# Performance work log

Hardware: AMD Instinct MI355X
Metric: run time of the kernel (lower is better)

Reference implementation:

```python
import jax, jax.numpy as jnp
import numpy as np

LN_EPS = 1e-5


def _layernorm(x, g, b):
    m = jnp.mean(x, axis=-1, keepdims=True)
    v = jnp.mean((x - m) ** 2, axis=-1, keepdims=True)
    return (x - m) / jnp.sqrt(v + LN_EPS) * g + b


def _eigenstate_fft(log_decay, frequency, beta_r, beta_i):
    # beta_r, beta_i: [B, T, K]; log_decay, frequency: [K]
    B, T, K = beta_r.shape
    mag = jax.nn.sigmoid(log_decay)                       # [K]
    n = jnp.arange(T, dtype=beta_r.dtype)                 # [T]
    mag_pow = mag[None, :] ** n[:, None]                  # [T, K]
    phase = n[:, None] * frequency[None, :]               # [T, K]
    kern = mag_pow * (jnp.cos(phase) + 1j * jnp.sin(phase))  # complex [T, K]
    beta = beta_r + 1j * beta_i                           # [B, T, K]
    beta_p = jnp.pad(beta, ((0, 0), (0, T), (0, 0)))      # zero-pad to 2T
    kern_p = jnp.pad(kern, ((0, T), (0, 0)))
    c = jnp.fft.ifft(jnp.fft.fft(beta_p, axis=1) * jnp.fft.fft(kern_p, axis=0)[None], axis=1)[:, :T, :]
    return c.real.astype(beta_r.dtype), c.imag.astype(beta_r.dtype)


def setup_inputs() -> dict:
    key = jax.random.key(0)
    ks = jax.random.split(key, 12)
    B, T, D, K, H = 4, 4096, 1024, 64, 4
    Kh = K // H
    M = 4 * D
    f32 = jnp.float32
    inp = {
        "x": jax.random.normal(ks[0], (B, T, D), f32),
        "in_proj_w": jax.random.normal(ks[1], (2 * K, D), f32) / np.sqrt(D),
        "log_decay": jax.random.uniform(ks[2], (K,), f32, -3.0, -0.1),
        "frequency": jnp.linspace(0.0, 2 * np.pi * (1 - 1.0 / K), K, dtype=f32),
        "coupling": jnp.eye(Kh, dtype=f32)[None] + 0.01 * jax.random.normal(ks[3], (H, Kh, Kh), f32) / np.sqrt(Kh),
        "out_proj_w": jax.random.normal(ks[4], (D, 2 * K), f32) / np.sqrt(2 * K),
        "gate_w": jax.random.normal(ks[5], (D, D), f32) / np.sqrt(D),
        "gate_b": jnp.full((D,), -2.0, f32),
        "n1_g": jnp.ones((D,), f32),
        "n1_b": jnp.zeros((D,), f32),
        "n2_g": jnp.ones((D,), f32),
        "n2_b": jnp.zeros((D,), f32),
        "mlp_w1": jax.random.normal(ks[6], (M, D), f32) / np.sqrt(D),
        "mlp_b1": jnp.zeros((M,), f32),
        "mlp_w2": jax.random.normal(ks[7], (D, M), f32) / np.sqrt(M),
        "mlp_b2": jnp.zeros((D,), f32),
    }
    return inp


def reference(x, in_proj_w, log_decay, frequency, coupling, out_proj_w,
              gate_w, gate_b, n1_g, n1_b, n2_g, n2_b,
              mlp_w1, mlp_b1, mlp_w2, mlp_b2):
    B, T, D = x.shape
    H, Kh, _ = coupling.shape
    K = H * Kh
    xn = _layernorm(x, n1_g, n1_b)
    beta = jnp.einsum('btd,kd->btk', xn, in_proj_w)        # [B, T, 2K]
    br, bi = beta[..., :K], beta[..., K:]
    cr, ci = _eigenstate_fft(log_decay, frequency, br, bi)  # [B, T, K] each
    cr_h = cr.reshape(B, T, H, Kh)
    ci_h = ci.reshape(B, T, H, Kh)
    cr = jnp.einsum('hjk,bthk->bthj', coupling, cr_h).reshape(B, T, K)
    ci = jnp.einsum('hjk,bthk->bthj', coupling, ci_h).reshape(B, T, K)
    eig = jnp.concatenate([cr, ci], axis=-1)               # [B, T, 2K]
    out = jnp.einsum('btk,dk->btd', eig, out_proj_w)
    h = jax.nn.sigmoid(jnp.einsum('btd,ed->bte', xn, gate_w) + gate_b) * out
    x = x + h                                              # dropout = identity (eval)
    x2 = _layernorm(x, n2_g, n2_b)
    hid = jax.nn.silu(jnp.einsum('btd,md->btm', x2, mlp_w1) + mlp_b1)
    x = x + jnp.einsum('btm,dm->btd', hid, mlp_w2) + mlp_b2
    return x, eig
```

## Files before the change

### kernel.cpp

```cpp
#include <hip/hip_runtime.h>
#include <hip/hip_bf16.h>
#include <math.h>

#define BATCH 4
#define TLEN  4096
#define DDIM  1024
#define BT    16384

typedef __attribute__((ext_vector_type(8))) __bf16 bf16x8;
typedef __attribute__((ext_vector_type(4))) float  f32x4;

#define AS1 __attribute__((address_space(1)))
#define AS3 __attribute__((address_space(3)))

__device__ __forceinline__ short f2bf(float f) {
    union { float f; unsigned int i; } u; u.f = f;
    unsigned int r = u.i + 0x7FFF + ((u.i >> 16) & 1);
    return (short)(r >> 16);
}

__global__ void cvt_bf16_kernel(const float* __restrict__ in, short* __restrict__ out, int n4) {
    int i = blockIdx.x * blockDim.x + threadIdx.x;
    int stride = gridDim.x * blockDim.x;
    for (; i < n4; i += stride) {
        float4 v = ((const float4*)in)[i];
        short4 o = make_short4(f2bf(v.x), f2bf(v.y), f2bf(v.z), f2bf(v.w));
        ((short4*)out)[i] = o;
    }
}

__global__ __launch_bounds__(256) void ln_kernel(const float* __restrict__ x,
                                                 const float* __restrict__ g,
                                                 const float* __restrict__ b,
                                                 short* __restrict__ out) {
    __shared__ float red[8];
    __shared__ float mv[2];
    int row = blockIdx.x, tid = threadIdx.x;
    const float* xr = x + (size_t)row * DDIM;
    float4 v = *(const float4*)&xr[tid * 4];
    float s  = v.x + v.y + v.z + v.w;
    float s2 = v.x*v.x + v.y*v.y + v.z*v.z + v.w*v.w;
    for (int o = 32; o; o >>= 1) { s += __shfl_down(s, o); s2 += __shfl_down(s2, o); }
    int wave = tid >> 6, lane = tid & 63;
    if (lane == 0) { red[wave] = s; red[4 + wave] = s2; }
    __syncthreads();
    if (tid == 0) {
        float ts  = red[0] + red[1] + red[2] + red[3];
        float ts2 = red[4] + red[5] + red[6] + red[7];
        float m = ts * (1.f / DDIM);
        float var = ts2 * (1.f / DDIM) - m * m;
        mv[0] = m; mv[1] = rsqrtf(var + 1e-5f);
    }
    __syncthreads();
    float m = mv[0], r = mv[1];
    const float* vv = (const float*)&v;
    short o4[4];
    #pragma unroll
    for (int j = 0; j < 4; ++j) {
        int c = tid * 4 + j;
        o4[j] = f2bf((vv[j] - m) * r * g[c] + b[c]);
    }
    *(short4*)&out[(size_t)row * DDIM + tid * 4] = make_short4(o4[0], o4[1], o4[2], o4[3]);
}

#define EIG_TT 16
#define WIN 64
__global__ __launch_bounds__(256) void eig_kernel(const float* __restrict__ beta,
                                                  const float* __restrict__ log_decay,
                                                  const float* __restrict__ freq,
                                                  const float* __restrict__ coupling,
                                                  float* __restrict__ eig_f32,
                                                  short* __restrict__ eig_bf) {
    __shared__ float bsm[EIG_TT + WIN][128];
    __shared__ float csm[EIG_TT][128];
    __shared__ float psm[4][16][16];
    int tpb = TLEN / EIG_TT;
    int b   = blockIdx.x / tpb;
    int t0  = (blockIdx.x % tpb) * EIG_TT;
    int tid = threadIdx.x;

    for (int idx = tid; idx < (EIG_TT + WIN) * 32; idx += 256) {
        int r = idx >> 5, c4 = idx & 31;
        int t = t0 - WIN + r;
        float4 val = make_float4(0.f, 0.f, 0.f, 0.f);
        if (t >= 0) val = *(const float4*)&beta[((size_t)(b * TLEN + t)) * 128 + c4 * 4];
        *(float4*)&bsm[r][c4 * 4] = val;
    }
    for (int i = tid; i < 1024; i += 256) ((float*)psm)[i] = coupling[i];
    __syncthreads();

    int k = tid & 63;
    float mag = 1.f / (1.f + __expf(-log_decay[k]));
    float th  = freq[k];
    float lr = mag * cosf(th), li = mag * sinf(th);
    #pragma unroll
    for (int p = 0; p < 4; ++p) {
        int tl = (tid >> 6) + p * 4;
        float ar = 0.f, ai = 0.f;
        for (int s = WIN - 1; s >= 0; --s) {
            float br_ = bsm[tl + WIN - s][k];
            float bi_ = bsm[tl + WIN - s][64 + k];
            float nr = lr * ar - li * ai + br_;
            float ni = lr * ai + li * ar + bi_;
            ar = nr; ai = ni;
        }
        csm[tl][k] = ar; csm[tl][64 + k] = ai;
    }
    __syncthreads();

    #pragma unroll
    for (int p = 0; p < 8; ++p) {
        int idx = tid + p * 256;
        int c = idx & 127, tl = idx >> 7;
        int im = c >> 6, hj = c & 63, h = hj >> 4, j = hj & 15;
        float acc = 0.f;
        #pragma unroll
        for (int kk = 0; kk < 16; ++kk) acc += psm[h][j][kk] * csm[tl][im * 64 + h * 16 + kk];
        size_t o = ((size_t)(b * TLEN + t0 + tl)) * 128 + c;
        eig_f32[o] = acc;
        eig_bf[o]  = f2bf(acc);
    }
}

__global__ __launch_bounds__(256) void gemm_bt(const short* __restrict__ A,
                                               const short* __restrict__ Bt,
                                               float* __restrict__ C,
                                               int Ndim, int Kdim) {
    __shared__ short Asm[128 * 32];
    __shared__ short Bsm[128 * 32];
    int nb = Ndim >> 7;
    int bm = blockIdx.x / nb, bn = blockIdx.x % nb;
    int m0 = bm << 7, n0 = bn << 7;
    int tid = threadIdx.x, lane = tid & 63, wave = tid >> 6;
    int wr = wave >> 1, wc = wave & 1;
    f32x4 acc[4][4] = {};
    int ldrow = lane >> 2;
    int ldcol = (lane & 3) * 8;
    int frow = lane & 15, fch = lane >> 4;

    for (int k0 = 0; k0 < Kdim; k0 += 32) {
        #pragma unroll
        for (int r = 0; r < 2; ++r) {
            int chunk = wave * 2 + r;
            int row = chunk * 16 + ldrow;
            __builtin_amdgcn_global_load_lds(
                (const AS1 unsigned int*)(A + (size_t)(m0 + row) * Kdim + k0 + ldcol),
                (AS3 unsigned int*)(Asm + chunk * 512 + lane * 8), 16, 0, 0);
            __builtin_amdgcn_global_load_lds(
                (const AS1 unsigned int*)(Bt + (size_t)(n0 + row) * Kdim + k0 + ldcol),
                (AS3 unsigned int*)(Bsm + chunk * 512 + lane * 8), 16, 0, 0);
        }
        __syncthreads();
        bf16x8 af[4], bf[4];
        #pragma unroll
        for (int m = 0; m < 4; ++m) af[m] = *(const bf16x8*)&Asm[(wr * 64 + m * 16 + frow) * 32 + fch * 8];
        #pragma unroll
        for (int n = 0; n < 4; ++n) bf[n] = *(const bf16x8*)&Bsm[(wc * 64 + n * 16 + frow) * 32 + fch * 8];
        #pragma unroll
        for (int m = 0; m < 4; ++m)
            #pragma unroll
            for (int n = 0; n < 4; ++n)
                acc[m][n] = __builtin_amdgcn_mfma_f32_16x16x32_bf16(af[m], bf[n], acc[m][n], 0, 0, 0);
        __syncthreads();
    }
    #pragma unroll
    for (int m = 0; m < 4; ++m) {
        int row = m0 + wr * 64 + m * 16 + fch * 4;
        #pragma unroll
        for (int n = 0; n < 4; ++n) {
            int col = n0 + wc * 64 + n * 16 + frow;
            #pragma unroll
            for (int j = 0; j < 4; ++j)
                C[(size_t)(row + j) * Ndim + col] = acc[m][n][j];
        }
    }
}

enum { E_NONE = 0, E_GATEFUSE = 1, E_SILU_BF = 2, E_RES = 3 };

#define BARRIER do { asm volatile("" ::: "memory"); __builtin_amdgcn_s_barrier(); } while (0)

#define STAGE(src, grow0, tau_, ldsShortBase) do { \
    int _i = tid; \
    _Pragma("unroll") \
    for (int _r = 0; _r < 2; ++_r, _i += 512) { \
        int _row = _i >> 3, _slot = _i & 7; \
        const short* _gp = (src) + (size_t)((grow0) + _row) * Kdim + ((tau_) << 6) \
                           + ((_slot ^ (_row & 7)) << 3); \
        __builtin_amdgcn_global_load_lds((const AS1 unsigned int*)_gp, \
            (AS3 unsigned int*)(lds + (ldsShortBase) + _i * 8), 16, 0, 0); \
    } \
} while (0)

#define LOAD_A(Ab, mq) do { \
    af0 = *(const bf16x8*)((Ab) + (2*(mq))  *2048 + lrb + x0); \
    af1 = *(const bf16x8*)((Ab) + (2*(mq))  *2048 + lrb + x1); \
    af2 = *(const bf16x8*)((Ab) + (2*(mq)+1)*2048 + lrb + x0); \
    af3 = *(const bf16x8*)((Ab) + (2*(mq)+1)*2048 + lrb + x1); \
} while (0)

#define PHASE_MFMA(mA, mB) do { \
    _Pragma("unroll") \
    for (int n = 0; n < 4; ++n) { \
        acc[mA][n] = __builtin_amdgcn_mfma_f32_16x16x32_bf16(af0, bfrag[n][0], acc[mA][n], 0, 0, 0); \
        acc[mA][n] = __builtin_amdgcn_mfma_f32_16x16x32_bf16(af1, bfrag[n][1], acc[mA][n], 0, 0, 0); \
        acc[mB][n] = __builtin_amdgcn_mfma_f32_16x16x32_bf16(af2, bfrag[n][0], acc[mB][n], 0, 0, 0); \
        acc[mB][n] = __builtin_amdgcn_mfma_f32_16x16x32_bf16(af3, bfrag[n][1], acc[mB][n], 0, 0, 0); \
    } \
} while (0)

#define KTILE(Ab, Bb, pB, pN, tau_) do { \
    bf16x8 af0, af1, af2, af3; \
     \
    LOAD_A(Ab, 0); \
    _Pragma("unroll") \
    for (int n = 0; n < 4; ++n) { \
        bfrag[n][0] = *(const bf16x8*)((Bb) + n * 2048 + lrb + x0); \
        bfrag[n][1] = *(const bf16x8*)((Bb) + n * 2048 + lrb + x1); \
    } \
    if ((tau_) + 1 < NT) STAGE(A, m0 + 128, (tau_) + 1, (pN) + 8192); \
    BARRIER; \
    __builtin_amdgcn_s_setprio(1); \
    PHASE_MFMA(0, 1); \
    __builtin_amdgcn_s_setprio(0); \
    BARRIER; \
     \
    LOAD_A(Ab, 1); \
    if ((tau_) + 2 < NT) STAGE(Bt, n0, (tau_) + 2, (pB) + 16384); \
    BARRIER; \
    __builtin_amdgcn_s_setprio(1); \
    PHASE_MFMA(2, 3); \
    __builtin_amdgcn_s_setprio(0); \
    BARRIER; \
     \
    LOAD_A(Ab, 2); \
    if ((tau_) + 2 < NT) STAGE(Bt, n0 + 128, (tau_) + 2, (pB) + 16384 + 8192); \
    BARRIER; \
    __builtin_amdgcn_s_setprio(1); \
    PHASE_MFMA(4, 5); \
    __builtin_amdgcn_s_setprio(0); \
    BARRIER; \
     \
    LOAD_A(Ab, 3); \
    BARRIER; \
    __builtin_amdgcn_s_setprio(1); \
    PHASE_MFMA(6, 7); \
    __builtin_amdgcn_s_setprio(0); \
    if ((tau_) + 2 < NT) { \
        STAGE(A, m0, (tau_) + 2, (pB)); \
        asm volatile("s_waitcnt vmcnt(6)" ::: "memory"); \
    } else { \
        asm volatile("s_waitcnt vmcnt(0)" ::: "memory"); \
    } \
    BARRIER; \
} while (0)

template <int EPI>
__global__ __launch_bounds__(512, 2) void gemm256(const short* __restrict__ A,
                                                  const short* __restrict__ Bt,
                                                  void* __restrict__ C,
                                                  int Ndim, int Kdim,
                                                  const float* __restrict__ bias,
                                                  const float* __restrict__ res,
                                                  const float* __restrict__ xin,
                                                  const float* __restrict__ outp) {
    __shared__ short lds[65536];
    const int NT = Kdim >> 6;
    const int nb = Ndim >> 8;
    int nwg = gridDim.x;
    int wg  = blockIdx.x;
    int swz = (wg & 7) * (nwg >> 3) + (wg >> 3);
    int bm = swz / nb, bn = swz % nb;
    int m0 = bm << 8, n0 = bn << 8;
    int tid = threadIdx.x, lane = tid & 63, wave = tid >> 6;
    int wr = wave >> 2, wc = wave & 3;
    int frow = lane & 15, fch = lane >> 4;

    f32x4 acc[8][4] = {};
    bf16x8 bfrag[4][2];

    int lrb = frow * 128;
    int sx  = frow & 7;
    int x0  = (fch ^ sx) << 4;
    int x1  = ((fch + 4) ^ sx) << 4;

    const char* Ab0 = (const char*)lds + wr * 16384;
    const char* Bb0 = (const char*)lds + 32768 + (wc >> 1) * 16384 + (wc & 1) * 8192;
    const char* Ab1 = Ab0 + 65536;
    const char* Bb1 = Bb0 + 65536;

    STAGE(Bt, n0,       0, 16384);
    STAGE(Bt, n0 + 128, 0, 16384 + 8192);
    STAGE(A,  m0,       0, 0);
    STAGE(A,  m0 + 128, 0, 8192);
    if (NT > 1) {
        STAGE(Bt, n0,       1, 32768 + 16384);
        STAGE(Bt, n0 + 128, 1, 32768 + 16384 + 8192);
        STAGE(A,  m0,       1, 32768);
    }
    asm volatile("s_waitcnt vmcnt(6)" ::: "memory");
    BARRIER;

    for (int tau = 0; tau < NT; tau += 2) {
        KTILE(Ab0, Bb0, 0,     32768, tau);
        KTILE(Ab1, Bb1, 32768, 0,     tau + 1);
    }

    #pragma unroll
    for (int m = 0; m < 8; ++m) {
        int row = m0 + wr * 128 + m * 16 + fch * 4;
        #pragma unroll
        for (int n = 0; n < 4; ++n) {
            int col = n0 + wc * 64 + n * 16 + frow;
            #pragma unroll
            for (int j = 0; j < 4; ++j) {
                float v = acc[m][n][j];
                size_t o = (size_t)(row + j) * Ndim + col;
                if (EPI == E_NONE) {
                    ((float*)C)[o] = v;
                } else if (EPI == E_GATEFUSE) {
                    float t = v + bias[col];
                    float s = 1.f / (1.f + __expf(-t));
                    ((float*)C)[o] = xin[o] + s * outp[o];
                } else if (EPI == E_SILU_BF) {
                    float t = v + bias[col];
                    ((short*)C)[o] = f2bf(t / (1.f + __expf(-t)));
                } else {
                    ((float*)C)[o] = v + bias[col] + res[o];
                }
            }
        }
    }
}

extern "C" void kernel_launch(void* const* d_in, const int* in_sizes, int n_in,
                              void* d_out, int out_size, void* d_ws, size_t ws_size,
                              hipStream_t stream) {
    const float* x          = (const float*)d_in[0];
    const float* in_proj_w  = (const float*)d_in[1];
    const float* log_decay  = (const float*)d_in[2];
    const float* frequency  = (const float*)d_in[3];
    const float* coupling   = (const float*)d_in[4];
    const float* out_proj_w = (const float*)d_in[5];
    const float* gate_w     = (const float*)d_in[6];
    const float* gate_b     = (const float*)d_in[7];
    const float* n1_g       = (const float*)d_in[8];
    const float* n1_b       = (const float*)d_in[9];
    const float* n2_g       = (const float*)d_in[10];
    const float* n2_b       = (const float*)d_in[11];
    const float* mlp_w1     = (const float*)d_in[12];
    const float* mlp_b1     = (const float*)d_in[13];
    const float* mlp_w2     = (const float*)d_in[14];
    const float* mlp_b2     = (const float*)d_in[15];

    float* out_x   = (float*)d_out;
    float* out_eig = out_x + (size_t)BT * DDIM;

    char* ws = (char*)d_ws;
    short* w_inproj  = (short*)(ws + 0);
    short* w_outproj = (short*)(ws + 262144);
    short* w_gate    = (short*)(ws + 524288);
    short* w_1       = (short*)(ws + 2621440);
    short* w_2       = (short*)(ws + 11010048);
    short* xn        = (short*)(ws + 19398656);
    float* beta      = (float*)(ws + 52953088);
    short* eig_bf    = (short*)(ws + 61341696);
    short* hid       = (short*)(ws + 65536000);
    float* outp      = (float*)(ws + 132644864);

    cvt_bf16_kernel<<<64,   256, 0, stream>>>(in_proj_w,  w_inproj,  131072 / 4);
    cvt_bf16_kernel<<<64,   256, 0, stream>>>(out_proj_w, w_outproj, 131072 / 4);
    cvt_bf16_kernel<<<256,  256, 0, stream>>>(gate_w,     w_gate,    1048576 / 4);
    cvt_bf16_kernel<<<1024, 256, 0, stream>>>(mlp_w1,     w_1,       4194304 / 4);
    cvt_bf16_kernel<<<1024, 256, 0, stream>>>(mlp_w2,     w_2,       4194304 / 4);

    ln_kernel<<<BT, 256, 0, stream>>>(x, n1_g, n1_b, xn);

    gemm_bt<<<BT / 128, 256, 0, stream>>>(xn, w_inproj, beta, 128, 1024);

    eig_kernel<<<BATCH * (TLEN / EIG_TT), 256, 0, stream>>>(beta, log_decay, frequency, coupling, out_eig, eig_bf);

    gemm256<E_NONE><<<(BT / 256) * (1024 / 256), 512, 0, stream>>>(
        eig_bf, w_outproj, outp, 1024, 128, nullptr, nullptr, nullptr, nullptr);

    gemm256<E_GATEFUSE><<<(BT / 256) * (1024 / 256), 512, 0, stream>>>(
        xn, w_gate, out_x, 1024, 1024, gate_b, nullptr, x, outp);

    ln_kernel<<<BT, 256, 0, stream>>>(out_x, n2_g, n2_b, xn);

    gemm256<E_SILU_BF><<<(BT / 256) * (4096 / 256), 512, 0, stream>>>(
        xn, w_1, hid, 4096, 1024, mlp_b1, nullptr, nullptr, nullptr);

    gemm256<E_RES><<<(BT / 256) * (1024 / 256), 512, 0, stream>>>(
        hid, w_2, out_x, 1024, 4096, mlp_b2, out_x, nullptr, nullptr);
}
```

Measured before the change: 630.0 us.

## Double-buffer A fragments and drop intra-phase barriers in GEMM k-tile loop

Splits A-fragment register reads into two ping-pong sets so the next quarter's LDS reads are issued before the current MFMA phase runs. It removes the barrier that sat between each LDS read and its MFMA phase, halving the barriers per k-tile. The last quarter's MFMAs are moved after the final A stage issue. This adds register pressure and depends on correct LDS hazard ordering, since stage writes may now overlap reads of the same buffer region.

```diff
diff --git a/kernel.cpp b/kernel.cpp
--- a/kernel.cpp
+++ b/kernel.cpp
@@ -192,64 +192,56 @@
     } \
 } while (0)
 
-#define LOAD_A(Ab, mq) do { \
-    af0 = *(const bf16x8*)((Ab) + (2*(mq))  *2048 + lrb + x0); \
-    af1 = *(const bf16x8*)((Ab) + (2*(mq))  *2048 + lrb + x1); \
-    af2 = *(const bf16x8*)((Ab) + (2*(mq)+1)*2048 + lrb + x0); \
-    af3 = *(const bf16x8*)((Ab) + (2*(mq)+1)*2048 + lrb + x1); \
+#define RD_AF(F, Ab, mq) do { \
+    F[0] = *(const bf16x8*)((Ab) + (2*(mq))  *2048 + lrb + x0); \
+    F[1] = *(const bf16x8*)((Ab) + (2*(mq))  *2048 + lrb + x1); \
+    F[2] = *(const bf16x8*)((Ab) + (2*(mq)+1)*2048 + lrb + x0); \
+    F[3] = *(const bf16x8*)((Ab) + (2*(mq)+1)*2048 + lrb + x1); \
 } while (0)
 
-#define PHASE_MFMA(mA, mB) do { \
+#define MFMA_Q(mA, mB, F) do { \
+    __builtin_amdgcn_s_setprio(1); \
     _Pragma("unroll") \
     for (int n = 0; n < 4; ++n) { \
-        acc[mA][n] = __builtin_amdgcn_mfma_f32_16x16x32_bf16(af0, bfrag[n][0], acc[mA][n], 0, 0, 0); \
-        acc[mA][n] = __builtin_amdgcn_mfma_f32_16x16x32_bf16(af1, bfrag[n][1], acc[mA][n], 0, 0, 0); \
-        acc[mB][n] = __builtin_amdgcn_mfma_f32_16x16x32_bf16(af2, bfrag[n][0], acc[mB][n], 0, 0, 0); \
-        acc[mB][n] = __builtin_amdgcn_mfma_f32_16x16x32_bf16(af3, bfrag[n][1], acc[mB][n], 0, 0, 0); \
+        acc[mA][n] = __builtin_amdgcn_mfma_f32_16x16x32_bf16(F[0], bfrag[n][0], acc[mA][n], 0, 0, 0); \
+        acc[mA][n] = __builtin_amdgcn_mfma_f32_16x16x32_bf16(F[1], bfrag[n][1], acc[mA][n], 0, 0, 0); \
+        acc[mB][n] = __builtin_amdgcn_mfma_f32_16x16x32_bf16(F[2], bfrag[n][0], acc[mB][n], 0, 0, 0); \
+        acc[mB][n] = __builtin_amdgcn_mfma_f32_16x16x32_bf16(F[3], bfrag[n][1], acc[mB][n], 0, 0, 0); \
     } \
+    __builtin_amdgcn_s_setprio(0); \
 } while (0)
 
 #define KTILE(Ab, Bb, pB, pN, tau_) do { \
-    bf16x8 af0, af1, af2, af3; \
+    bf16x8 afA[4], afB[4]; \
      \
-    LOAD_A(Ab, 0); \
+    RD_AF(afA, Ab, 0); \
     _Pragma("unroll") \
     for (int n = 0; n < 4; ++n) { \
         bfrag[n][0] = *(const bf16x8*)((Bb) + n * 2048 + lrb + x0); \
         bfrag[n][1] = *(const bf16x8*)((Bb) + n * 2048 + lrb + x1); \
     } \
+    RD_AF(afB, Ab, 1); \
     if ((tau_) + 1 < NT) STAGE(A, m0 + 128, (tau_) + 1, (pN) + 8192); \
-    BARRIER; \
-    __builtin_amdgcn_s_setprio(1); \
-    PHASE_MFMA(0, 1); \
-    __builtin_amdgcn_s_setprio(0); \
+    MFMA_Q(0, 1, afA); \
     BARRIER; \
      \
-    LOAD_A(Ab, 1); \
+    RD_AF(afA, Ab, 2); \
     if ((tau_) + 2 < NT) STAGE(Bt, n0, (tau_) + 2, (pB) + 16384); \
-    BARRIER; \
-    __builtin_amdgcn_s_setprio(1); \
-    PHASE_MFMA(2, 3); \
-    __builtin_amdgcn_s_setprio(0); \
+    MFMA_Q(2, 3, afB); \
     BARRIER; \
      \
-    LOAD_A(Ab, 2); \
+    RD_AF(afB, Ab, 3); \
     if ((tau_) + 2 < NT) STAGE(Bt, n0 + 128, (tau_) + 2, (pB) + 16384 + 8192); \
-    BARRIER; \
-    __builtin_amdgcn_s_setprio(1); \
-    PHASE_MFMA(4, 5); \
-    __builtin_amdgcn_s_setprio(0); \
+    MFMA_Q(4, 5, afA); \
+    asm volatile("s_waitcnt lgkmcnt(0)" ::: "memory"); \
     BARRIER; \
      \
-    LOAD_A(Ab, 3); \
-    BARRIER; \
-    __builtin_amdgcn_s_setprio(1); \
-    PHASE_MFMA(6, 7); \
-    __builtin_amdgcn_s_setprio(0); \
     if ((tau_) + 2 < NT) { \
         STAGE(A, m0, (tau_) + 2, (pB)); \
+        MFMA_Q(6, 7, afB); \
         asm volatile("s_waitcnt vmcnt(6)" ::: "memory"); \
     } else { \
+        MFMA_Q(6, 7, afB); \
         asm volatile("s_waitcnt vmcnt(0)" ::: "memory"); \
     } \
     BARRIER; \
```

Measured after the change: 617.7 us. About the same (-1.9%).
